# Kernel tuning notes

Measured on AMD Instinct MI355X. Metric: run time of the kernel, lower is better.

Reference implementation:

```python
import jax, jax.numpy as jnp
import numpy as np

B, S, EMB, H = 2, 2048, 1024, 16
D = EMB // H  # per-head dim = 64
SCALE = 1.0 / np.sqrt(D).astype(np.float32)


def setup_inputs() -> dict:
    key = jax.random.key(0)
    ks = jax.random.split(key, 11)
    lim = 1.0 / np.sqrt(EMB).astype(np.float32)  # torch Linear default init range
    def lin(kw, kb):
        W = jax.random.uniform(kw, (EMB, EMB), jnp.float32, -lim, lim)
        b = jax.random.uniform(kb, (EMB,), jnp.float32, -lim, lim)
        return W, b
    Wq, bq = lin(ks[0], ks[1])
    Wk, bk = lin(ks[2], ks[3])
    Wv, bv = lin(ks[4], ks[5])
    Wo, bo = lin(ks[6], ks[7])
    xq = jax.random.normal(ks[8], (B, S, EMB), jnp.float32)
    xk = jax.random.normal(ks[9], (B, S, EMB), jnp.float32)
    xv = jax.random.normal(ks[10], (B, S, EMB), jnp.float32)
    mask = jnp.tril(jnp.ones((S, S), dtype=jnp.int32))  # causal mask; 0 -> blocked
    return {"xq": xq, "xk": xk, "xv": xv, "mask": mask,
            "Wq": Wq, "bq": bq, "Wk": Wk, "bk": bk,
            "Wv": Wv, "bv": bv, "Wo": Wo, "bo": bo}


def reference(xq, xk, xv, mask, Wq, bq, Wk, bk, Wv, bv, Wo, bo):
    # Projections (torch Linear: x @ W.T + b), then split heads: [B,S,E] -> [B,H,S,D]
    def split_heads(x):
        return x.reshape(B, S, H, D).transpose(0, 2, 1, 3)
    Q = split_heads(xq @ Wq.T + bq)
    K = split_heads(xk @ Wk.T + bk)
    V = split_heads(xv @ Wv.T + bv)
    scores = jnp.einsum("bhqd,bhkd->bhqk", Q, K) * SCALE  # [B,H,S,S]
    scores = jnp.where(mask[None, None, :, :] == 0, jnp.float32(-1e9), scores)
    attn = jax.nn.softmax(scores, axis=-1)  # softmax over key axis (dim=2 per-head in torch)
    res = jnp.einsum("bhqk,bhkd->bhqd", attn, V)
    res = res.transpose(0, 2, 1, 3).reshape(B, S, EMB)  # merge heads back (same slicing layout)
    return res @ Wo.T + bo
```

## Files before the change

### kernel.cpp

```cpp
#include <hip/hip_runtime.h>
#include <hip/hip_bf16.h>

#define BB   2
#define SS   2048
#define EMBD 1024
#define NH   16
#define HD   64
#define QSCALE 0.18033688011112042f
#define NEG_BIG (-1e30f)

typedef __bf16 bf16;
typedef float  floatx4 __attribute__((ext_vector_type(4)));
typedef __bf16 bf16x4  __attribute__((ext_vector_type(4)));
typedef __bf16 bf16x8  __attribute__((ext_vector_type(8)));

typedef const __attribute__((address_space(1))) void* gas_ptr;
typedef __attribute__((address_space(3))) void*       las_ptr;

__device__ __forceinline__ void gl_lds16(const void* g, void* l) {
    __builtin_amdgcn_global_load_lds((gas_ptr)g, (las_ptr)l, 16, 0, 0);
}

__device__ __forceinline__ bf16x8 cvt8(const float* p) {
    bf16x8 o;
#pragma unroll
    for (int j = 0; j < 8; j++) o[j] = (bf16)p[j];
    return o;
}

__global__ __launch_bounds__(256) void cvt_all(
    const float* __restrict__ xq, const float* __restrict__ xk,
    const float* __restrict__ xv, const float* __restrict__ Wq,
    const float* __restrict__ Wk, const float* __restrict__ Wv,
    const float* __restrict__ Wo, bf16* __restrict__ xqo,
    bf16* __restrict__ xko, bf16* __restrict__ xvo, bf16* __restrict__ Wqo,
    bf16* __restrict__ Wko, bf16* __restrict__ Wvo, bf16* __restrict__ Woo) {
    const int y = blockIdx.y;
    const float* src;
    bf16* dst;
    size_t n;
    const size_t NX = (size_t)BB * SS * EMBD;
    const size_t NW = (size_t)EMBD * EMBD;
    switch (y) {
        case 0: src = xq; dst = xqo; n = NX; break;
        case 1: src = xk; dst = xko; n = NX; break;
        case 2: src = xv; dst = xvo; n = NX; break;
        case 3: src = Wq; dst = Wqo; n = NW; break;
        case 4: src = Wk; dst = Wko; n = NW; break;
        case 5: src = Wv; dst = Wvo; n = NW; break;
        default: src = Wo; dst = Woo; n = NW; break;
    }
    const size_t stride = (size_t)gridDim.x * blockDim.x * 4;
    for (size_t i = ((size_t)blockIdx.x * blockDim.x + threadIdx.x) * 4;
         i < n; i += stride) {
        floatx4 v = *(const floatx4*)(src + i);
        bf16x4 o = {(bf16)v[0], (bf16)v[1], (bf16)v[2], (bf16)v[3]};
        *(bf16x4*)(dst + i) = o;
    }
}

extern __shared__ __align__(16) char smem[];

template <int MODE, int FM>
__device__ __forceinline__ void gemm_body(const bf16* __restrict__ A,
                                          const bf16* __restrict__ W,
                                          const float* __restrict__ bias,
                                          void* __restrict__ Ov,
                                          int mBase, int nBase, float oscale) {
    constexpr int BM = 32 * FM;
    constexpr int ABYTES = BM * 64 * 2;
    bf16* As = (bf16*)smem;
    bf16* Bs = (bf16*)(smem + ABYTES);

    const int t = threadIdx.x;
    const int l = t & 63, w = t >> 6;
    const int lm = l & 15, lq = l >> 4;
    const int K = 1024;
    const int wm = (w >> 1) * (16 * FM), wn = (w & 1) * 64;

    const floatx4 zero = {0.f, 0.f, 0.f, 0.f};
    floatx4 acc[FM][4];
#pragma unroll
    for (int i = 0; i < FM; i++)
#pragma unroll
        for (int j = 0; j < 4; j++) acc[i][j] = zero;

    for (int kb = 0; kb < K; kb += 64) {
        __syncthreads();
#pragma unroll
        for (int ia = 0; ia < FM; ia++) {
            int half = ia / (FM / 2 > 0 ? FM / 2 : 1);
            int rem  = (ia % (FM / 2 > 0 ? FM / 2 : 1)) * 256 + t;
            int row  = rem >> 2;
            int col  = half * 32 + (rem & 3) * 8;
            gl_lds16(A + (size_t)(mBase + row) * K + kb + col,
                     (char*)As + (ia * 256 + w * 64) * 16);
        }
#pragma unroll
        for (int i = 0; i < 4; i++) {
            int half = i >> 1;
            int rem  = (i & 1) * 256 + t;
            int row  = rem >> 2;
            int col  = half * 32 + (rem & 3) * 8;
            gl_lds16(W + (size_t)(nBase + row) * K + kb + col,
                     (char*)Bs + (i * 256 + w * 64) * 16);
        }
        __syncthreads();

#pragma unroll
        for (int half = 0; half < 2; half++) {
            const bf16* Ah = As + half * BM * 32;
            const bf16* Bh = Bs + half * 128 * 32;
            bf16x8 af[FM], bfv[4];
#pragma unroll
            for (int f = 0; f < FM; f++)
                af[f] = *(const bf16x8*)&Ah[(wm + f * 16 + lm) * 32 + lq * 8];
#pragma unroll
            for (int f = 0; f < 4; f++)
                bfv[f] = *(const bf16x8*)&Bh[(wn + f * 16 + lm) * 32 + lq * 8];
            if (MODE == 2) {
#pragma unroll
                for (int i = 0; i < 4; i++)
#pragma unroll
                    for (int j = 0; j < FM; j++)
                        acc[j][i] = __builtin_amdgcn_mfma_f32_16x16x32_bf16(
                            bfv[i], af[j], acc[j][i], 0, 0, 0);
            } else {
#pragma unroll
                for (int fm = 0; fm < FM; fm++)
#pragma unroll
                    for (int fn = 0; fn < 4; fn++)
                        acc[fm][fn] =
                            __builtin_amdgcn_mfma_f32_16x16x32_bf16(
                                af[fm], bfv[fn], acc[fm][fn], 0, 0, 0);
            }
        }
    }

    __syncthreads();
    float* rp = (float*)smem + w * (16 * 68);

    if (MODE != 2) {
        float bvv[4];
#pragma unroll
        for (int fn = 0; fn < 4; fn++)
            bvv[fn] = bias[nBase + wn + fn * 16 + lm];
#pragma unroll
        for (int fm = 0; fm < FM; fm++) {
#pragma unroll
            for (int fn = 0; fn < 4; fn++)
#pragma unroll
                for (int r = 0; r < 4; r++)
                    rp[(lq * 4 + r) * 68 + fn * 16 + lm] =
                        (acc[fm][fn][r] + bvv[fn]) * oscale;
            if (MODE == 0) {
                int row2 = l >> 3, col8 = l & 7;
                int h = (nBase + wn) >> 6;
#pragma unroll
                for (int p = 0; p < 2; p++) {
                    int row = p * 8 + row2;
                    int m = mBase + wm + fm * 16 + row;
                    int b = m >> 11, s = m & 2047;
                    bf16x8 o = cvt8(&rp[row * 68 + col8 * 8]);
                    *(bf16x8*)((bf16*)Ov +
                               (((size_t)(b * NH + h)) * SS + s) * HD +
                               col8 * 8) = o;
                }
            } else {
                int c4 = l & 15;
#pragma unroll
                for (int p = 0; p < 4; p++) {
                    int row = p * 4 + (l >> 4);
                    int m = mBase + wm + fm * 16 + row;
                    floatx4 o = *(const floatx4*)&rp[row * 68 + c4 * 4];
                    *(floatx4*)((float*)Ov + (size_t)m * EMBD + nBase + wn +
                                c4 * 4) = o;
                }
            }
        }
    } else {
        const int b = (mBase + wm) >> 11;
        const int sbase = (mBase + wm) & 2047;
#pragma unroll
        for (int i = 0; i < 4; i++) {
            float bv[4];
#pragma unroll
            for (int r = 0; r < 4; r++)
                bv[r] = bias[nBase + wn + i * 16 + lq * 4 + r];
#pragma unroll
            for (int j = 0; j < FM; j++)
#pragma unroll
                for (int r = 0; r < 4; r++)
                    rp[(lq * 4 + r) * 68 + j * 16 + lm] =
                        acc[j][i][r] + bv[r];
            int row2 = l >> 3, col8 = l & 7;
#pragma unroll
            for (int p = 0; p < 2; p++) {
                int row = p * 8 + row2;
                int n = nBase + wn + i * 16 + row;
                int h = n >> 6, d = n & 63;
                bf16x8 o = cvt8(&rp[row * 68 + col8 * 8]);
                *(bf16x8*)((bf16*)Ov +
                           ((size_t)(b * NH + h) * HD + d) * SS + sbase +
                           col8 * 8) = o;
            }
        }
    }
}

__global__ __launch_bounds__(256, 4) void gemm_qkv(
    const bf16* __restrict__ xq, const bf16* __restrict__ xk,
    const bf16* __restrict__ xv, const bf16* __restrict__ Wq,
    const bf16* __restrict__ Wk, const bf16* __restrict__ Wv,
    const float* __restrict__ bq, const float* __restrict__ bk,
    const float* __restrict__ bv, bf16* __restrict__ Qo,
    bf16* __restrict__ Ko, bf16* __restrict__ Vo) {
    const int z = blockIdx.z;
    const int mB = blockIdx.x * 128, nB = blockIdx.y * 128;
    if (z == 0)
        gemm_body<0, 4>(xq, Wq, bq, Qo, mB, nB, QSCALE);
    else if (z == 1)
        gemm_body<0, 4>(xk, Wk, bk, Ko, mB, nB, 1.0f);
    else
        gemm_body<2, 4>(xv, Wv, bv, Vo, mB, nB, 1.0f);
}

__global__ __launch_bounds__(256, 4) void gemm_out(
    const bf16* __restrict__ A, const bf16* __restrict__ W,
    const float* __restrict__ bias, float* __restrict__ O) {
    gemm_body<1, 2>(A, W, bias, O, blockIdx.x * 64, blockIdx.y * 128, 1.0f);
}

__global__ __launch_bounds__(256, 3) void attn_fwd(
    const bf16* __restrict__ Qg, const bf16* __restrict__ Kg,
    const bf16* __restrict__ Vtg, bf16* __restrict__ Oatt) {
    __shared__ __align__(16) bf16 Ks[128 * 72];
    __shared__ __align__(16) bf16 VT[64 * 136];
    __shared__ __align__(16) bf16 Ps[4][16 * 136];

    const int t = threadIdx.x;
    const int l = t & 63, w = t >> 6;
    const int lm = l & 15, lq = l >> 4;
    const int x = blockIdx.x;
    const int qt = 31 - (x >> 5);
    const int bh = (((x >> 3) & 3) << 3) | (x & 7);
    const int nch = (qt >> 1) + 1;
    const size_t kbase = (size_t)bh * SS * HD;
    const size_t vbase = (size_t)bh * HD * SS;
    const int b = bh >> 4, h = bh & 15;
    const floatx4 zero = {0.f, 0.f, 0.f, 0.f};

    bf16x8 qa0, qa1;
    {
        const bf16* qp =
            Qg + kbase + (size_t)(qt * 64 + w * 16 + lm) * HD + lq * 8;
        qa0 = *(const bf16x8*)qp;
        qa1 = *(const bf16x8*)(qp + 32);
    }

    float m_i = NEG_BIG, l_i = 0.f;
    floatx4 od[4];
#pragma unroll
    for (int dt = 0; dt < 4; dt++) od[dt] = zero;

    const int qglob = qt * 64 + w * 16 + lm;

    bf16x8 kreg[4], vreg[4];
#pragma unroll
    for (int i = 0; i < 4; i++) {
        int idx = i * 256 + t;
        int rowK = idx >> 3, colK = (idx & 7) * 8;
        kreg[i] = *(const bf16x8*)(Kg + kbase + (size_t)rowK * HD + colK);
        int dV = idx >> 4, keyb = (idx & 15) * 8;
        vreg[i] = *(const bf16x8*)(Vtg + vbase + (size_t)dV * SS + keyb);
    }

    for (int kt = 0; kt < nch; ++kt) {
        __syncthreads();
#pragma unroll
        for (int i = 0; i < 4; i++) {
            int idx = i * 256 + t;
            int rowK = idx >> 3, colK = (idx & 7) * 8;
            *(bf16x8*)&Ks[rowK * 72 + colK] = kreg[i];
            int dV = idx >> 4, keyb = (idx & 15) * 8;
            *(bf16x8*)&VT[dV * 136 + keyb] = vreg[i];
        }
        __syncthreads();
        if (kt < nch - 1) {
#pragma unroll
            for (int i = 0; i < 4; i++) {
                int idx = i * 256 + t;
                int rowK = idx >> 3, colK = (idx & 7) * 8;
                kreg[i] = *(const bf16x8*)(
                    Kg + kbase + (size_t)((kt + 1) * 128 + rowK) * HD + colK);
                int dV = idx >> 4, keyb = (idx & 15) * 8;
                vreg[i] = *(const bf16x8*)(
                    Vtg + vbase + (size_t)dV * SS + (kt + 1) * 128 + keyb);
            }
        }

        floatx4 sc[8];
#pragma unroll
        for (int j0 = 0; j0 < 8; j0++) {
            int rowK = j0 * 16 + lm;
            bf16x8 k0 = *(const bf16x8*)&Ks[rowK * 72 + lq * 8];
            bf16x8 k1 = *(const bf16x8*)&Ks[rowK * 72 + 32 + lq * 8];
            floatx4 z = zero;
            z = __builtin_amdgcn_mfma_f32_16x16x32_bf16(k0, qa0, z, 0, 0, 0);
            z = __builtin_amdgcn_mfma_f32_16x16x32_bf16(k1, qa1, z, 0, 0, 0);
            sc[j0] = z;
        }
        if (kt == nch - 1) {
#pragma unroll
            for (int j0 = 0; j0 < 8; j0++)
#pragma unroll
                for (int r = 0; r < 4; r++) {
                    int key = kt * 128 + j0 * 16 + lq * 4 + r;
                    if (key > qglob) sc[j0][r] = NEG_BIG;
                }
        }
        float mt = sc[0][0];
#pragma unroll
        for (int j0 = 0; j0 < 8; j0++)
#pragma unroll
            for (int r = 0; r < 4; r++) mt = fmaxf(mt, sc[j0][r]);
        mt = fmaxf(mt, __shfl_xor(mt, 16));
        mt = fmaxf(mt, __shfl_xor(mt, 32));
        float mnew = fmaxf(m_i, mt);
        float alpha = __builtin_amdgcn_exp2f(m_i - mnew);
        m_i = mnew;
        float ps = 0.f;
#pragma unroll
        for (int j0 = 0; j0 < 8; j0++)
#pragma unroll
            for (int r = 0; r < 4; r++) {
                float p = __builtin_amdgcn_exp2f(sc[j0][r] - mnew);
                sc[j0][r] = p;
                ps += p;
            }
        ps += __shfl_xor(ps, 16);
        ps += __shfl_xor(ps, 32);
        l_i = l_i * alpha + ps;
#pragma unroll
        for (int j0 = 0; j0 < 8; j0++) {
            bf16x4 pk = {(bf16)sc[j0][0], (bf16)sc[j0][1], (bf16)sc[j0][2],
                         (bf16)sc[j0][3]};
            *(bf16x4*)&Ps[w][lm * 136 + j0 * 16 + lq * 4] = pk;
        }
        float a0 = __shfl(alpha, lq * 4 + 0);
        float a1 = __shfl(alpha, lq * 4 + 1);
        float a2 = __shfl(alpha, lq * 4 + 2);
        float a3 = __shfl(alpha, lq * 4 + 3);
#pragma unroll
        for (int dt = 0; dt < 4; dt++) {
            od[dt][0] *= a0;
            od[dt][1] *= a1;
            od[dt][2] *= a2;
            od[dt][3] *= a3;
        }
        bf16x8 pa[4];
#pragma unroll
        for (int s = 0; s < 4; s++)
            pa[s] = *(const bf16x8*)&Ps[w][lm * 136 + s * 32 + lq * 8];
#pragma unroll
        for (int dt = 0; dt < 4; dt++) {
            int rowD = dt * 16 + lm;
#pragma unroll
            for (int s = 0; s < 4; s++) {
                bf16x8 v = *(const bf16x8*)&VT[rowD * 136 + s * 32 + lq * 8];
                od[dt] = __builtin_amdgcn_mfma_f32_16x16x32_bf16(pa[s], v,
                                                                 od[dt], 0, 0,
                                                                 0);
            }
        }
    }

    float linv = 1.0f / l_i;
    float lr0 = __shfl(linv, lq * 4 + 0);
    float lr1 = __shfl(linv, lq * 4 + 1);
    float lr2 = __shfl(linv, lq * 4 + 2);
    float lr3 = __shfl(linv, lq * 4 + 3);
    float lr[4] = {lr0, lr1, lr2, lr3};
#pragma unroll
    for (int dt = 0; dt < 4; dt++) {
#pragma unroll
        for (int r = 0; r < 4; r++) {
            int s = qt * 64 + w * 16 + lq * 4 + r;
            float v = od[dt][r] * lr[r];
            Oatt[((size_t)(b * SS + s)) * EMBD + h * HD + dt * 16 + lm] =
                (bf16)v;
        }
    }
}

extern "C" void kernel_launch(void* const* d_in, const int* in_sizes, int n_in,
                              void* d_out, int out_size, void* d_ws,
                              size_t ws_size, hipStream_t stream) {
    const float* xq = (const float*)d_in[0];
    const float* xk = (const float*)d_in[1];
    const float* xv = (const float*)d_in[2];
    const float* Wq = (const float*)d_in[4];
    const float* bq = (const float*)d_in[5];
    const float* Wk = (const float*)d_in[6];
    const float* bk = (const float*)d_in[7];
    const float* Wv = (const float*)d_in[8];
    const float* bv = (const float*)d_in[9];
    const float* Wo = (const float*)d_in[10];
    const float* bo = (const float*)d_in[11];
    float* out = (float*)d_out;

    const size_t NX = (size_t)BB * SS * EMBD;
    const size_t NW = (size_t)EMBD * EMBD;
    bf16* Qw  = (bf16*)d_ws;
    bf16* Kw  = Qw + NX;
    bf16* Vw  = Kw + NX;
    bf16* Aw  = Vw + NX;
    bf16* xqb = Aw + NX;
    bf16* xkb = xqb + NX;
    bf16* xvb = xkb + NX;
    bf16* Wqb = xvb + NX;
    bf16* Wkb = Wqb + NW;
    bf16* Wvb = Wkb + NW;
    bf16* Wob = Wvb + NW;

    cvt_all<<<dim3(1024, 7), 256, 0, stream>>>(xq, xk, xv, Wq, Wk, Wv, Wo,
                                               xqb, xkb, xvb, Wqb, Wkb, Wvb,
                                               Wob);
    gemm_qkv<<<dim3(32, 8, 3), 256, 32768, stream>>>(
        xqb, xkb, xvb, Wqb, Wkb, Wvb, bq, bk, bv, Qw, Kw, Vw);
    attn_fwd<<<dim3(1024), 256, 0, stream>>>(Qw, Kw, Vw, Aw);
    gemm_out<<<dim3(64, 8), 256, 24576, stream>>>(Aw, Wob, bo, out);
}
```

Measured before the change: 219.6 us.

## Swizzle attention LDS layouts, halve P staging, and rebalance q-tile ordering

Replaces padded LDS tiles for K, V^T and P with XOR-swizzled unpadded layouts, which shrinks shared memory so the launch bound can be raised from 3 to 4 blocks per CU. P is now staged in two 64-key halves interleaved with the PV MFMAs, which halves the per-wave P buffer. The q-tile order is permuted so long and short causal tiles are mixed across the grid to balance load. The max and sum reductions are split into parallel trees to shorten dependency chains. Swizzle index math adds ALU work, and the raised occupancy target may cause register spills.

```diff
diff --git a/kernel.cpp b/kernel.cpp
--- a/kernel.cpp
+++ b/kernel.cpp
@@ -231,18 +231,24 @@
     gemm_body<1, 2>(A, W, bias, O, blockIdx.x * 64, blockIdx.y * 128, 1.0f);
 }
 
-__global__ __launch_bounds__(256, 3) void attn_fwd(
+__global__ __launch_bounds__(256, 4) void attn_fwd(
     const bf16* __restrict__ Qg, const bf16* __restrict__ Kg,
     const bf16* __restrict__ Vtg, bf16* __restrict__ Oatt) {
-    __shared__ __align__(16) bf16 Ks[128 * 72];
-    __shared__ __align__(16) bf16 VT[64 * 136];
-    __shared__ __align__(16) bf16 Ps[4][16 * 136];
+    __shared__ __align__(16) bf16 Ks[128 * 64];
+    __shared__ __align__(16) bf16 VT[64 * 128];
+    __shared__ __align__(16) bf16 Ps[4][16 * 64];
 
     const int t = threadIdx.x;
     const int l = t & 63, w = t >> 6;
     const int lm = l & 15, lq = l >> 4;
+    const int m7 = lm & 7;
     const int x = blockIdx.x;
-    const int qt = 31 - (x >> 5);
+    const int i5 = x >> 5;
+    const int gq = i5 >> 3, jq = i5 & 7;
+    const int qt = (gq == 0) ? jq
+                 : (gq == 1) ? 15 - jq
+                 : (gq == 2) ? 16 + jq
+                             : 31 - jq;
     const int bh = (((x >> 3) & 3) << 3) | (x & 7);
     const int nch = (qt >> 1) + 1;
     const size_t kbase = (size_t)bh * SS * HD;
@@ -280,10 +286,11 @@
 #pragma unroll
         for (int i = 0; i < 4; i++) {
             int idx = i * 256 + t;
-            int rowK = idx >> 3, colK = (idx & 7) * 8;
-            *(bf16x8*)&Ks[rowK * 72 + colK] = kreg[i];
-            int dV = idx >> 4, keyb = (idx & 15) * 8;
-            *(bf16x8*)&VT[dV * 136 + keyb] = vreg[i];
+            int rowK = idx >> 3, c16 = idx & 7;
+            *(bf16x8*)&Ks[rowK * 64 + ((c16 ^ (rowK & 7)) << 3)] = kreg[i];
+            int dV = idx >> 4, k16 = idx & 15;
+            *(bf16x8*)&VT[dV * 128 +
+                          (((k16 & 8) | ((k16 ^ dV) & 7)) << 3)] = vreg[i];
         }
         __syncthreads();
         if (kt < nch - 1) {
@@ -303,8 +310,9 @@
 #pragma unroll
         for (int j0 = 0; j0 < 8; j0++) {
             int rowK = j0 * 16 + lm;
-            bf16x8 k0 = *(const bf16x8*)&Ks[rowK * 72 + lq * 8];
-            bf16x8 k1 = *(const bf16x8*)&Ks[rowK * 72 + 32 + lq * 8];
+            bf16x8 k0 = *(const bf16x8*)&Ks[rowK * 64 + ((lq ^ m7) << 3)];
+            bf16x8 k1 =
+                *(const bf16x8*)&Ks[rowK * 64 + (((4 + lq) ^ m7) << 3)];
             floatx4 z = zero;
             z = __builtin_amdgcn_mfma_f32_16x16x32_bf16(k0, qa0, z, 0, 0, 0);
             z = __builtin_amdgcn_mfma_f32_16x16x32_bf16(k1, qa1, z, 0, 0, 0);
@@ -319,34 +327,36 @@
                     if (key > qglob) sc[j0][r] = NEG_BIG;
                 }
         }
-        float mt = sc[0][0];
-#pragma unroll
-        for (int j0 = 0; j0 < 8; j0++)
-#pragma unroll
-            for (int r = 0; r < 4; r++) mt = fmaxf(mt, sc[j0][r]);
+        float m4[4];
+#pragma unroll
+        for (int a = 0; a < 4; a++) {
+            float u0 = fmaxf(fmaxf(sc[a][0], sc[a][1]),
+                             fmaxf(sc[a][2], sc[a][3]));
+            float u1 = fmaxf(fmaxf(sc[a + 4][0], sc[a + 4][1]),
+                             fmaxf(sc[a + 4][2], sc[a + 4][3]));
+            m4[a] = fmaxf(u0, u1);
+        }
+        float mt = fmaxf(fmaxf(m4[0], m4[1]), fmaxf(m4[2], m4[3]));
         mt = fmaxf(mt, __shfl_xor(mt, 16));
         mt = fmaxf(mt, __shfl_xor(mt, 32));
         float mnew = fmaxf(m_i, mt);
         float alpha = __builtin_amdgcn_exp2f(m_i - mnew);
         m_i = mnew;
-        float ps = 0.f;
-#pragma unroll
-        for (int j0 = 0; j0 < 8; j0++)
-#pragma unroll
-            for (int r = 0; r < 4; r++) {
-                float p = __builtin_amdgcn_exp2f(sc[j0][r] - mnew);
-                sc[j0][r] = p;
-                ps += p;
-            }
+        float psa0 = 0.f, psa1 = 0.f, psa2 = 0.f, psa3 = 0.f;
+#pragma unroll
+        for (int j0 = 0; j0 < 8; j0++) {
+            float p0 = __builtin_amdgcn_exp2f(sc[j0][0] - mnew);
+            float p1 = __builtin_amdgcn_exp2f(sc[j0][1] - mnew);
+            float p2 = __builtin_amdgcn_exp2f(sc[j0][2] - mnew);
+            float p3 = __builtin_amdgcn_exp2f(sc[j0][3] - mnew);
+            sc[j0][0] = p0; sc[j0][1] = p1;
+            sc[j0][2] = p2; sc[j0][3] = p3;
+            psa0 += p0; psa1 += p1; psa2 += p2; psa3 += p3;
+        }
+        float ps = (psa0 + psa1) + (psa2 + psa3);
         ps += __shfl_xor(ps, 16);
         ps += __shfl_xor(ps, 32);
         l_i = l_i * alpha + ps;
-#pragma unroll
-        for (int j0 = 0; j0 < 8; j0++) {
-            bf16x4 pk = {(bf16)sc[j0][0], (bf16)sc[j0][1], (bf16)sc[j0][2],
-                         (bf16)sc[j0][3]};
-            *(bf16x4*)&Ps[w][lm * 136 + j0 * 16 + lq * 4] = pk;
-        }
         float a0 = __shfl(alpha, lq * 4 + 0);
         float a1 = __shfl(alpha, lq * 4 + 1);
         float a2 = __shfl(alpha, lq * 4 + 2);
@@ -358,17 +368,33 @@
             od[dt][2] *= a2;
             od[dt][3] *= a3;
         }
-        bf16x8 pa[4];
-#pragma unroll
-        for (int s = 0; s < 4; s++)
-            pa[s] = *(const bf16x8*)&Ps[w][lm * 136 + s * 32 + lq * 8];
-#pragma unroll
-        for (int dt = 0; dt < 4; dt++) {
-            int rowD = dt * 16 + lm;
-#pragma unroll
-            for (int s = 0; s < 4; s++) {
-                bf16x8 v = *(const bf16x8*)&VT[rowD * 136 + s * 32 + lq * 8];
-                od[dt] = __builtin_amdgcn_mfma_f32_16x16x32_bf16(pa[s], v,
+#pragma unroll
+        for (int hv = 0; hv < 2; hv++) {
+#pragma unroll
+            for (int j0l = 0; j0l < 4; j0l++) {
+                floatx4 s4 = sc[hv * 4 + j0l];
+                bf16x4 pk = {(bf16)s4[0], (bf16)s4[1], (bf16)s4[2],
+                             (bf16)s4[3]};
+                *(bf16x4*)&Ps[w][lm * 64 +
+                                 ((j0l * 16 + lq * 4) ^ (m7 * 8))] = pk;
+            }
+            bf16x8 pa0 =
+                *(const bf16x8*)&Ps[w][lm * 64 + ((lq * 8) ^ (m7 * 8))];
+            bf16x8 pa1 =
+                *(const bf16x8*)&Ps[w][lm * 64 + ((32 + lq * 8) ^ (m7 * 8))];
+#pragma unroll
+            for (int dt = 0; dt < 4; dt++) {
+                int rowD = dt * 16 + lm;
+                int sl0 = hv * 8 + lq;
+                int sl1 = sl0 + 4;
+                bf16x8 v0 = *(const bf16x8*)&VT[
+                    rowD * 128 + (((sl0 & 8) | ((sl0 ^ m7) & 7)) << 3)];
+                od[dt] = __builtin_amdgcn_mfma_f32_16x16x32_bf16(pa0, v0,
+                                                                 od[dt], 0, 0,
+                                                                 0);
+                bf16x8 v1 = *(const bf16x8*)&VT[
+                    rowD * 128 + (((sl1 & 8) | ((sl1 ^ m7) & 7)) << 3)];
+                od[dt] = __builtin_amdgcn_mfma_f32_16x16x32_bf16(pa1, v1,
                                                                  od[dt], 0, 0,
                                                                  0);
             }
```

New measurement: 249.3 us. 1.14x slower.
